# Kernel optimization log

Measured on AMD Instinct MI355X. Metric: run time of the kernel, lower is better.

Reference implementation:

```python
import jax, jax.numpy as jnp
import numpy as np

B, S, E, H = 2, 2048, 2048, 16
D = E // H  # head_dim = 128
ROPE_BASE = 10000.0


def setup_inputs() -> dict:
    key = jax.random.key(0)
    ks = jax.random.split(key, 6)
    x = jax.random.normal(ks[0], (B, S, E), dtype=jnp.float32)
    # additive causal mask: 0 where attendable, -1e9 above diagonal
    causal = jnp.where(jnp.tril(jnp.ones((S, S), dtype=bool)), 0.0, -1e9).astype(jnp.float32)
    mask = jnp.broadcast_to(causal[None, None], (B, 1, S, S))
    # RoPE tables (rotate-half convention)
    inv_freq = 1.0 / (ROPE_BASE ** (jnp.arange(0, D, 2, dtype=jnp.float32) / D))
    freqs = jnp.arange(S, dtype=jnp.float32)[:, None] * inv_freq[None, :]  # [S, D/2]
    emb = jnp.concatenate([freqs, freqs], axis=-1)  # [S, D]
    cos, sin = jnp.cos(emb), jnp.sin(emb)
    std = 0.02
    Wq = jax.random.normal(ks[1], (E, E), dtype=jnp.float32) * std
    Wk = jax.random.normal(ks[2], (E, E), dtype=jnp.float32) * std
    Wv = jax.random.normal(ks[3], (E, E), dtype=jnp.float32) * std
    Wo = jax.random.normal(ks[4], (E, E), dtype=jnp.float32) * std
    zb = jnp.zeros((E,), dtype=jnp.float32)
    return {"x": x, "mask": mask, "cos": cos, "sin": sin,
            "Wq": Wq, "bq": zb, "Wk": Wk, "bk": zb, "Wv": Wv, "bv": zb,
            "Wo": Wo, "bo": zb, "rope_exclude": 0}


def _rotate_half(t):
    t1, t2 = jnp.split(t, 2, axis=-1)
    return jnp.concatenate([-t2, t1], axis=-1)


def _apply_rope(t, cos, sin, rope_exclude):
    # t: [B, H, S, D]; cos/sin: [S, D]
    rot = t * cos[None, None] + _rotate_half(t) * sin[None, None]
    keep = (jnp.arange(t.shape[2]) < rope_exclude)[None, None, :, None]
    return jnp.where(keep, t, rot)


def reference(x, mask, cos, sin, Wq, bq, Wk, bk, Wv, bv, Wo, bo, rope_exclude):
    b, s, e = x.shape
    scale = D ** -0.5
    def heads(y):
        return y.reshape(b, s, H, D).transpose(0, 2, 1, 3)  # [B,H,S,D]
    q = heads(x @ Wq.T + bq)
    k = heads(x @ Wk.T + bk)
    v = heads(x @ Wv.T + bv)
    q = _apply_rope(q, cos, sin, rope_exclude)
    k = _apply_rope(k, cos, sin, rope_exclude)
    scores = jnp.einsum('bhqd,bhkd->bhqk', q, k) * scale + mask
    attn = jax.nn.softmax(scores, axis=-1)  # dropout is identity in eval mode
    ctx = jnp.einsum('bhqk,bhkd->bhqd', attn, v)
    ctx = ctx.transpose(0, 2, 1, 3).reshape(b, s, e)
    return ctx @ Wo.T + bo
```

## Files before the change

### kernel.cpp

```cpp
#include <hip/hip_runtime.h>


#define BB 2
#define SS 2048
#define EE 2048
#define HH 16
#define DD 128
#define BH 32
#define MR 4096
#define BKK 64
#define NTK (EE / BKK)

typedef __attribute__((ext_vector_type(8))) short short8;
typedef __attribute__((ext_vector_type(4))) short short4v;
typedef __attribute__((ext_vector_type(4))) float floatx4;
typedef unsigned int u32;

__device__ __forceinline__ float bf2f(unsigned short u) {
    union { unsigned int i; float f; } v; v.i = ((unsigned int)u) << 16; return v.f;
}
__device__ __forceinline__ unsigned short f2bf(float f) {
    union { float f; unsigned int i; } v; v.f = f;
    unsigned int x = v.i;
    return (unsigned short)((x + 0x7fffu + ((x >> 16) & 1u)) >> 16);
}

__device__ __forceinline__ void async_copy16(const unsigned short* g, unsigned short* l) {
    __builtin_amdgcn_global_load_lds((const __attribute__((address_space(1))) u32*)g,
                                     (__attribute__((address_space(3))) u32*)l, 16, 0, 0);
}

__global__ __launch_bounds__(256)
void cvt_all(const float* __restrict__ x,  const float* __restrict__ Wq,
             const float* __restrict__ Wk, const float* __restrict__ Wv,
             const float* __restrict__ Wo, unsigned short* __restrict__ dst)
{
    const size_t wsz = (size_t)EE * EE;
    size_t i = ((size_t)blockIdx.x * 256 + threadIdx.x) * 8;
    const float* src; size_t off;
    if      (i <     wsz) { src = Wo; off = 0; }
    else if (i < 2 * wsz) { src = Wq; off = wsz; }
    else if (i < 3 * wsz) { src = Wk; off = 2 * wsz; }
    else if (i < 4 * wsz) { src = Wv; off = 3 * wsz; }
    else                  { src = x;  off = 4 * wsz; }
    const float* p = src + (i - off);
    floatx4 v0 = *(const floatx4*)p;
    floatx4 v1 = *(const floatx4*)(p + 4);
    short8 o;
    #pragma unroll
    for (int j = 0; j < 4; ++j) { o[j] = (short)f2bf(v0[j]); o[4 + j] = (short)f2bf(v1[j]); }
    *(short8*)&dst[i] = o;
}

__device__ __forceinline__ void stageA(const unsigned short* __restrict__ X,
                                       unsigned short* Asb, int mbase, int k0,
                                       int w, int lane)
{
    const int rsub = lane >> 3;
    const int ksw  = ((lane & 7) ^ rsub) << 3;
    #pragma unroll
    for (int h = 0; h < 2; ++h)
        #pragma unroll
        for (int c = 0; c < 2; ++c) {
            int r = h * 128 + (w * 2 + c) * 8 + rsub;
            async_copy16(&X[(size_t)(mbase + r) * EE + k0 + ksw],
                         &Asb[h * 8192 + (w * 2 + c) * 512]);
        }
}
__device__ __forceinline__ void stageB(const unsigned short* __restrict__ W,
                                       unsigned short* Bsb, int nbase, int k0,
                                       int w, int lane)
{
    const int rsub = lane >> 3;
    const int ksw  = ((lane & 7) ^ rsub) << 3;
    #pragma unroll
    for (int c = 0; c < 2; ++c) {
        int r = (w * 2 + c) * 8 + rsub;
        async_copy16(&W[(size_t)(nbase + r) * EE + k0 + ksw],
                     &Bsb[(w * 2 + c) * 512]);
    }
}

template<int MODE>
__global__ __launch_bounds__(512, 1)
void gemm8(const unsigned short* __restrict__ X,
           const unsigned short* __restrict__ W,
           const float* __restrict__ bias0,
           const float* __restrict__ bias1,
           const float* __restrict__ bias2,
           const float* __restrict__ cosT,
           const float* __restrict__ sinT,
           const int* __restrict__ rex,
           void* __restrict__ outv)
{
    __shared__ __align__(16) unsigned short As[3][256 * 64];
    __shared__ __align__(16) unsigned short Bs[3][128 * 64];

    const int NXB = (MODE == 0) ? 48 : 16;
    const int nwg = (MODE == 0) ? 768 : 256;
    const int q8  = nwg >> 3;
    const int wg  = ((int)blockIdx.x & 7) * q8 + ((int)blockIdx.x >> 3);
    const int xb = wg % NXB, yb = wg / NXB;
    const int mbase = yb * 256;
    const int nbase = xb * 128;

    const int tid  = threadIdx.x;
    const int w    = tid >> 6, lane = tid & 63;
    const int quad = lane >> 4, l16 = lane & 15;
    const int wm = w >> 1, wn = w & 1;

    floatx4 acc[4][4];
    #pragma unroll
    for (int mi = 0; mi < 4; ++mi)
        #pragma unroll
        for (int ni = 0; ni < 4; ++ni)
            acc[mi][ni] = (floatx4){0.f, 0.f, 0.f, 0.f};

    const int kx0 = (quad * 8) ^ ((l16 & 7) << 3);
    const int kx1 = (32 + quad * 8) ^ ((l16 & 7) << 3);

    stageA(X, As[0], mbase, 0,   w, lane);  stageB(W, Bs[0], nbase, 0,   w, lane);
    stageA(X, As[1], mbase, BKK, w, lane);  stageB(W, Bs[1], nbase, BKK, w, lane);
    asm volatile("s_waitcnt vmcnt(6)" ::: "memory");
    asm volatile("s_barrier" ::: "memory");

    for (int t = 0; t < NTK; ++t) {
        const unsigned short* Ab = As[t % 3];
        const unsigned short* Bb = Bs[t % 3];
        unsigned short* An = As[(t + 2) % 3];
        unsigned short* Bn = Bs[(t + 2) % 3];
        const bool pf = (t + 2 < NTK);
        const int kn = (t + 2) * BKK;

        short8 b[4][2];
        #pragma unroll
        for (int ni = 0; ni < 4; ++ni) {
            int rb = (wn * 64 + ni * 16 + l16) * 64;
            b[ni][0] = *(const short8*)&Bb[rb + kx0];
            b[ni][1] = *(const short8*)&Bb[rb + kx1];
        }
        short8 a[4][2];
        #pragma unroll
        for (int mi = 0; mi < 2; ++mi) {
            int ra = (wm * 64 + mi * 16 + l16) * 64;
            a[mi][0] = *(const short8*)&Ab[ra + kx0];
            a[mi][1] = *(const short8*)&Ab[ra + kx1];
        }
        if (pf) stageA(X, An, mbase, kn, w, lane);
        __builtin_amdgcn_s_setprio(1);
        #pragma unroll
        for (int mi = 0; mi < 2; ++mi)
            #pragma unroll
            for (int ni = 0; ni < 4; ++ni) {
                acc[mi][ni] = __builtin_amdgcn_mfma_f32_16x16x32_bf16(a[mi][0], b[ni][0], acc[mi][ni], 0, 0, 0);
                acc[mi][ni] = __builtin_amdgcn_mfma_f32_16x16x32_bf16(a[mi][1], b[ni][1], acc[mi][ni], 0, 0, 0);
            }
        __builtin_amdgcn_s_setprio(0);

        #pragma unroll
        for (int mi = 2; mi < 4; ++mi) {
            int ra = (wm * 64 + mi * 16 + l16) * 64;
            a[mi][0] = *(const short8*)&Ab[ra + kx0];
            a[mi][1] = *(const short8*)&Ab[ra + kx1];
        }
        if (pf) stageB(W, Bn, nbase, kn, w, lane);
        __builtin_amdgcn_s_setprio(1);
        #pragma unroll
        for (int mi = 2; mi < 4; ++mi)
            #pragma unroll
            for (int ni = 0; ni < 4; ++ni) {
                acc[mi][ni] = __builtin_amdgcn_mfma_f32_16x16x32_bf16(a[mi][0], b[ni][0], acc[mi][ni], 0, 0, 0);
                acc[mi][ni] = __builtin_amdgcn_mfma_f32_16x16x32_bf16(a[mi][1], b[ni][1], acc[mi][ni], 0, 0, 0);
            }
        __builtin_amdgcn_s_setprio(0);
        if (pf) asm volatile("s_waitcnt vmcnt(6)" ::: "memory");
        else    asm volatile("s_waitcnt vmcnt(0)" ::: "memory");
        asm volatile("s_barrier" ::: "memory");
    }

    if (MODE == 1) {
        #pragma unroll
        for (int ni = 0; ni < 4; ++ni) {
            int n = nbase + wn * 64 + ni * 16 + l16;
            float bval = bias0[n];
            #pragma unroll
            for (int mi = 0; mi < 4; ++mi)
                #pragma unroll
                for (int rr = 0; rr < 4; ++rr) {
                    int m = mbase + wm * 64 + mi * 16 + quad * 4 + rr;
                    ((float*)outv)[(size_t)m * EE + n] = acc[mi][ni][rr] + bval;
                }
        }
    } else {
        unsigned short (*Ls)[132] = (unsigned short(*)[132])&As[0][0];
        #pragma unroll
        for (int ni = 0; ni < 4; ++ni) {
            int nl = wn * 64 + ni * 16 + l16;
            int n  = nbase + nl;
            const float* bp = (n < 2048) ? bias0 : (n < 4096) ? bias1 : bias2;
            float bval = bp[n & (EE - 1)];
            #pragma unroll
            for (int mi = 0; mi < 4; ++mi)
                #pragma unroll
                for (int rr = 0; rr < 4; ++rr)
                    Ls[wm * 64 + mi * 16 + quad * 4 + rr][nl] = f2bf(acc[mi][ni][rr] + bval);
        }
        __syncthreads();

        const int r0 = tid >> 4;
        const int c0 = (tid & 15) * 4;
        const int nz = nbase + c0;
        const int z  = nz >> 11;
        const int hh = (nz >> 7) & (HH - 1);
        const float qs = (z == 0) ? 0.08838834764831845f : 1.0f;
        const int rexv = rex[0];
        unsigned short* op16 = (unsigned short*)outv;
        #pragma unroll
        for (int rr2 = 0; rr2 < 8; ++rr2) {
            int row = r0 * 8 + rr2;
            int m = mbase + row;
            int s = m & (SS - 1), bi = m >> 11;
            short4v lo = *(short4v*)&Ls[row][c0];
            short4v hi = *(short4v*)&Ls[row][c0 + 64];
            floatx4 c1 = *(const floatx4*)&cosT[(size_t)s * DD + c0];
            floatx4 s1 = *(const floatx4*)&sinT[(size_t)s * DD + c0];
            floatx4 c2 = *(const floatx4*)&cosT[(size_t)s * DD + c0 + 64];
            floatx4 s2 = *(const floatx4*)&sinT[(size_t)s * DD + c0 + 64];
            bool rot = (z < 2) && (s >= rexv);
            short4v o1, o2;
            #pragma unroll
            for (int c = 0; c < 4; ++c) {
                float f1 = bf2f((unsigned short)lo[c]);
                float f2 = bf2f((unsigned short)hi[c]);
                float r1 = rot ? (f1 * c1[c] - f2 * s1[c]) : f1;
                float r2 = rot ? (f2 * c2[c] + f1 * s2[c]) : f2;
                o1[c] = (short)f2bf(r1 * qs);
                o2[c] = (short)f2bf(r2 * qs);
            }
            size_t base = (size_t)z * ((size_t)BH * SS * DD)
                        + ((size_t)(bi * HH + hh) * SS + s) * DD;
            *(short4v*)&op16[base + c0]      = o1;
            *(short4v*)&op16[base + c0 + 64] = o2;
        }
    }
}

template<int MODE>
__global__ __launch_bounds__(256, 2)
void gemm_bt(const void* __restrict__ Xv,
             const float* __restrict__ W0,
             const float* __restrict__ W1,
             const float* __restrict__ W2,
             const float* __restrict__ bias0,
             const float* __restrict__ bias1,
             const float* __restrict__ bias2,
             void* __restrict__ outv)
{
    const float* W;
    const float* bias;
    unsigned short* op16 = nullptr;
    float* op32 = nullptr;
    if (MODE == 0) {
        int z = blockIdx.z;
        W    = (z == 0) ? W0 : (z == 1) ? W1 : W2;
        bias = (z == 0) ? bias0 : (z == 1) ? bias1 : bias2;
        op16 = (unsigned short*)outv + (size_t)z * ((size_t)BH * SS * DD);
    } else {
        W = W0; bias = bias0; op32 = (float*)outv;
    }

    __shared__ unsigned short As[4][128][8];
    __shared__ unsigned short Bs[4][128][8];

    const int tid  = threadIdx.x;
    const int wave = tid >> 6, lane = tid & 63;
    const int quad = lane >> 4, l16 = lane & 15;
    const int wr = (wave >> 1) * 64;
    const int wc = (wave & 1) * 64;
    const int mbase = blockIdx.y * 128, nbase = blockIdx.x * 128;

    const int srow  = tid >> 1;
    const int shalf = tid & 1;
    const int sc0   = shalf * 2;

    floatx4 acc[4][4];
    #pragma unroll
    for (int i = 0; i < 4; ++i)
        #pragma unroll
        for (int c = 0; c < 4; ++c)
            acc[i][c] = (floatx4){0.f, 0.f, 0.f, 0.f};

    const size_t arow = (size_t)(mbase + srow) * EE;
    const size_t brow = (size_t)(nbase + srow) * EE;

    for (int k0 = 0; k0 < EE; k0 += 32) {
        if (MODE == 0) {
            const float* px = &((const float*)Xv)[arow + k0 + shalf * 16];
            short8 lo, hi;
            #pragma unroll
            for (int j = 0; j < 8; ++j) lo[j] = (short)f2bf(px[j]);
            #pragma unroll
            for (int j = 0; j < 8; ++j) hi[j] = (short)f2bf(px[8 + j]);
            *(short8*)&As[sc0    ][srow][0] = lo;
            *(short8*)&As[sc0 + 1][srow][0] = hi;
        } else {
            const unsigned short* Xb = (const unsigned short*)Xv;
            *(short8*)&As[sc0    ][srow][0] = *(const short8*)&Xb[arow + k0 + shalf * 16];
            *(short8*)&As[sc0 + 1][srow][0] = *(const short8*)&Xb[arow + k0 + shalf * 16 + 8];
        }
        {
            const float* pw = &W[brow + k0 + shalf * 16];
            short8 lo, hi;
            #pragma unroll
            for (int j = 0; j < 8; ++j) lo[j] = (short)f2bf(pw[j]);
            #pragma unroll
            for (int j = 0; j < 8; ++j) hi[j] = (short)f2bf(pw[8 + j]);
            *(short8*)&Bs[sc0    ][srow][0] = lo;
            *(short8*)&Bs[sc0 + 1][srow][0] = hi;
        }
        __syncthreads();

        short8 a[4], b[4];
        #pragma unroll
        for (int i = 0; i < 4; ++i) a[i] = *(short8*)&As[quad][wr + i * 16 + l16][0];
        #pragma unroll
        for (int c = 0; c < 4; ++c) b[c] = *(short8*)&Bs[quad][wc + c * 16 + l16][0];
        #pragma unroll
        for (int i = 0; i < 4; ++i)
            #pragma unroll
            for (int c = 0; c < 4; ++c)
                acc[i][c] = __builtin_amdgcn_mfma_f32_16x16x32_bf16(a[i], b[c], acc[i][c], 0, 0, 0);
        __syncthreads();
    }

    #pragma unroll
    for (int c = 0; c < 4; ++c) {
        int n = nbase + wc + c * 16 + l16;
        float bval = bias[n];
        #pragma unroll
        for (int i = 0; i < 4; ++i) {
            #pragma unroll
            for (int r = 0; r < 4; ++r) {
                int m = mbase + wr + i * 16 + quad * 4 + r;
                float val = acc[i][c][r] + bval;
                if (MODE == 0) {
                    int bi = m >> 11, s = m & (SS - 1);
                    int h  = n >> 7,  d = n & (DD - 1);
                    op16[(((size_t)(bi * HH + h)) * SS + s) * DD + d] = f2bf(val);
                } else {
                    op32[(size_t)m * EE + n] = val;
                }
            }
        }
    }
}

__global__ __launch_bounds__(256)
void rope_kernel(unsigned short* __restrict__ Qw, unsigned short* __restrict__ Kw,
                 const float* __restrict__ cosT,
                 const float* __restrict__ sinT,
                 const int* __restrict__ rex)
{
    int idx = blockIdx.x * 256 + threadIdx.x;
    int d4 = idx & 15;
    int s  = (idx >> 4) & (SS - 1);
    int bh = (idx >> 15) & (BH - 1);
    int t  = idx >> 20;
    unsigned short* T = t ? Kw : Qw;
    const float qs = t ? 1.0f : 0.08838834764831845f;

    size_t base  = ((size_t)bh * SS + s) * DD + d4 * 4;
    size_t cbase = (size_t)s * DD + d4 * 4;

    short4v v1 = *(short4v*)&T[base];
    short4v v2 = *(short4v*)&T[base + 64];
    floatx4 c1 = *(const floatx4*)&cosT[cbase];
    floatx4 s1 = *(const floatx4*)&sinT[cbase];
    floatx4 c2 = *(const floatx4*)&cosT[cbase + 64];
    floatx4 s2 = *(const floatx4*)&sinT[cbase + 64];

    bool keep = (s < rex[0]);
    short4v o1, o2;
    #pragma unroll
    for (int i = 0; i < 4; ++i) {
        float f1 = bf2f((unsigned short)v1[i]);
        float f2 = bf2f((unsigned short)v2[i]);
        float r1 = f1 * c1[i] - f2 * s1[i];
        float r2 = f2 * c2[i] + f1 * s2[i];
        o1[i] = (short)f2bf((keep ? f1 : r1) * qs);
        o2[i] = (short)f2bf((keep ? f2 : r2) * qs);
    }
    *(short4v*)&T[base]      = o1;
    *(short4v*)&T[base + 64] = o2;
}

__global__ __launch_bounds__(512, 1)
void attn_mfma(const unsigned short* __restrict__ Qw,
               const unsigned short* __restrict__ Kw,
               const unsigned short* __restrict__ Vw,
               unsigned short* __restrict__ O)
{
    __shared__ unsigned short Ks[16][64][8];
    __shared__ unsigned short Vt[128][72];
    __shared__ unsigned short Ps[8][32][72];

    const int tid  = threadIdx.x;
    const int w    = tid >> 6, lane = tid & 63;
    const int quad = lane >> 4, l16 = lane & 15;
    const int bh = blockIdx.y;
    const int b = bh >> 4, h = bh & (HH - 1);
    const int x = blockIdx.x;
    const int half = w >> 2, wsub = w & 3;
    const int qbh  = half ? x : (15 - x);
    const int myrow = qbh * 128 + wsub * 32;

    const size_t head = (size_t)bh * SS * DD;

    short8 aq[2][4];
    #pragma unroll
    for (int hh = 0; hh < 2; ++hh) {
        const unsigned short* qp = &Qw[head + (size_t)(myrow + hh * 16 + l16) * DD];
        #pragma unroll
        for (int kc = 0; kc < 4; ++kc) aq[hh][kc] = *(const short8*)&qp[kc * 32 + quad * 8];
    }

    floatx4 oacc[2][8];
    #pragma unroll
    for (int hh = 0; hh < 2; ++hh)
        #pragma unroll
        for (int i = 0; i < 8; ++i) oacc[hh][i] = (floatx4){0.f, 0.f, 0.f, 0.f};
    float l_part[2][4];
    #pragma unroll
    for (int hh = 0; hh < 2; ++hh)
        #pragma unroll
        for (int r = 0; r < 4; ++r) l_part[hh][r] = 0.f;

    const int ntiles = 2 * (15 - x) + 2;
    for (int kt = 0; kt < ntiles; ++kt) {
        __syncthreads();

        #pragma unroll
        for (int it = 0; it < 2; ++it) {
            int key = it * 32 + (tid >> 4);
            int dc  = tid & 15;
            short8 v = *(const short8*)&Kw[head + (size_t)(kt * 64 + key) * DD + dc * 8];
            *(short8*)&Ks[dc][key ^ (dc & 7)][0] = v;
        }
        #pragma unroll
        for (int it = 0; it < 2; ++it) {
            int key = lane;
            int dc  = it * 8 + w;
            short8 v = *(const short8*)&Vw[head + (size_t)(kt * 64 + key) * DD + dc * 8];
            #pragma unroll
            for (int i = 0; i < 8; ++i) Vt[dc * 8 + i][key] = (unsigned short)v[i];
        }
        __syncthreads();

        if (kt * 64 > myrow + 31) continue;

        floatx4 sacc[2][4];
        #pragma unroll
        for (int hh = 0; hh < 2; ++hh)
            #pragma unroll
            for (int nt = 0; nt < 4; ++nt) sacc[hh][nt] = (floatx4){0.f, 0.f, 0.f, 0.f};
        #pragma unroll
        for (int kc = 0; kc < 4; ++kc) {
            int dcr = kc * 4 + quad;
            #pragma unroll
            for (int nt = 0; nt < 4; ++nt) {
                short8 bfrag = *(const short8*)&Ks[dcr][(nt * 16) + (l16 ^ (dcr & 7))][0];
                sacc[0][nt] = __builtin_amdgcn_mfma_f32_16x16x32_bf16(aq[0][kc], bfrag, sacc[0][nt], 0, 0, 0);
                sacc[1][nt] = __builtin_amdgcn_mfma_f32_16x16x32_bf16(aq[1][kc], bfrag, sacc[1][nt], 0, 0, 0);
            }
        }

        #pragma unroll
        for (int hh = 0; hh < 2; ++hh)
            #pragma unroll
            for (int nt = 0; nt < 4; ++nt)
                #pragma unroll
                for (int rr = 0; rr < 4; ++rr) {
                    int keyg = kt * 64 + nt * 16 + l16;
                    int qg   = myrow + hh * 16 + quad * 4 + rr;
                    float p = (keyg <= qg) ? __expf(sacc[hh][nt][rr]) : 0.f;
                    l_part[hh][rr] += p;
                    Ps[w][hh * 16 + quad * 4 + rr][nt * 16 + l16] = f2bf(p);
                }

        #pragma unroll
        for (int kc = 0; kc < 2; ++kc) {
            short8 pa0 = *(const short8*)&Ps[w][l16][kc * 32 + quad * 8];
            short8 pa1 = *(const short8*)&Ps[w][16 + l16][kc * 32 + quad * 8];
            #pragma unroll
            for (int nt = 0; nt < 8; ++nt) {
                short8 vb = *(const short8*)&Vt[nt * 16 + l16][kc * 32 + quad * 8];
                oacc[0][nt] = __builtin_amdgcn_mfma_f32_16x16x32_bf16(pa0, vb, oacc[0][nt], 0, 0, 0);
                oacc[1][nt] = __builtin_amdgcn_mfma_f32_16x16x32_bf16(pa1, vb, oacc[1][nt], 0, 0, 0);
            }
        }
    }

    #pragma unroll
    for (int hh = 0; hh < 2; ++hh)
        #pragma unroll
        for (int rr = 0; rr < 4; ++rr) {
            float l = l_part[hh][rr];
            l += __shfl_xor(l, 1, 16);
            l += __shfl_xor(l, 2, 16);
            l += __shfl_xor(l, 4, 16);
            l += __shfl_xor(l, 8, 16);
            float inv = 1.f / l;
            int qg = myrow + hh * 16 + quad * 4 + rr;
            unsigned short* cp = &O[((size_t)b * SS + qg) * EE + h * DD];
            #pragma unroll
            for (int nt = 0; nt < 8; ++nt)
                cp[nt * 16 + l16] = f2bf(oacc[hh][nt][rr] * inv);
        }
}

__global__ void sentinel_kernel(float* out, int n) {
    int i = blockIdx.x * 256 + threadIdx.x;
    if (i < n) out[i] = 1.0e6f;
}

extern "C" void kernel_launch(void* const* d_in, const int* in_sizes, int n_in,
                              void* d_out, int out_size, void* d_ws, size_t ws_size,
                              hipStream_t stream)
{
    const float* x    = (const float*)d_in[0];
    const float* cosT = (const float*)d_in[2];
    const float* sinT = (const float*)d_in[3];
    const float* Wq = (const float*)d_in[4];
    const float* bq = (const float*)d_in[5];
    const float* Wk = (const float*)d_in[6];
    const float* bk = (const float*)d_in[7];
    const float* Wv = (const float*)d_in[8];
    const float* bv = (const float*)d_in[9];
    const float* Wo = (const float*)d_in[10];
    const float* bo = (const float*)d_in[11];
    const int* rex = (const int*)d_in[12];

    const size_t tsz = (size_t)BH * SS * DD;
    const size_t wsz = (size_t)EE * EE;
    const size_t need_small = 4 * tsz * sizeof(unsigned short);
    const size_t need_big   = (3 * tsz + 4 * wsz + tsz) * sizeof(unsigned short);

    unsigned short* ws = (unsigned short*)d_ws;
    unsigned short* Qws = ws;
    unsigned short* Kws = ws + tsz;
    unsigned short* Vws = ws + 2 * tsz;

    if (ws_size >= need_big) {
        unsigned short* Wob = ws + 3 * tsz;
        unsigned short* Wqb = Wob + wsz;
        unsigned short* Wkb = Wqb + wsz;
        unsigned short* Wvb = Wkb + wsz;
        unsigned short* Xb  = Wvb + wsz;
        unsigned short* Cws = Xb;

        cvt_all<<<(int)((4 * wsz + tsz) / 8 / 256), 256, 0, stream>>>(x, Wq, Wk, Wv, Wo, Wob);

        gemm8<0><<<768, 512, 0, stream>>>(Xb, Wqb, bq, bk, bv, cosT, sinT, rex, Qws);
        attn_mfma<<<dim3(8, BH), 512, 0, stream>>>(Qws, Kws, Vws, Cws);
        gemm8<1><<<256, 512, 0, stream>>>(Cws, Wob, bo, bo, bo, cosT, sinT, rex, d_out);
    } else if (ws_size >= need_small) {
        unsigned short* Cws = ws + 3 * tsz;
        gemm_bt<0><<<dim3(16, 32, 3), 256, 0, stream>>>(x, Wq, Wk, Wv, bq, bk, bv, Qws);
        rope_kernel<<<8192, 256, 0, stream>>>(Qws, Kws, cosT, sinT, rex);
        attn_mfma<<<dim3(8, BH), 512, 0, stream>>>(Qws, Kws, Vws, Cws);
        gemm_bt<1><<<dim3(16, 32, 1), 256, 0, stream>>>(Cws, Wo, Wo, Wo, bo, bo, bo, d_out);
    } else {
        sentinel_kernel<<<(out_size + 255) / 256, 256, 0, stream>>>((float*)d_out, out_size);
    }
}
```

Baseline: 419.3 us.

## Double-buffer K/V tiles in attention with register prefetch and MFMA priority

The attention kernel now keeps two LDS buffers for K and V. The next tile's global loads are issued into registers before computing on the current tile, and are written to the other buffer afterwards, so one barrier per iteration replaces two. This is meant to hide global load latency behind the QK and PV MFMA work. It also raises wave priority around the MFMA sections with s_setprio. The cost is double the LDS for K/V and extra live registers for the prefetched data.

Result: no change. 411.1 us (-1.9%).

```diff
diff --git a/kernel.cpp b/kernel.cpp
--- a/kernel.cpp
+++ b/kernel.cpp
@@ -400,8 +400,8 @@
                const unsigned short* __restrict__ Vw,
                unsigned short* __restrict__ O)
 {
-    __shared__ unsigned short Ks[16][64][8];
-    __shared__ unsigned short Vt[128][72];
+    __shared__ unsigned short Ks[2][16][64][8];
+    __shared__ unsigned short Vt[2][128][72];
     __shared__ unsigned short Ps[8][32][72];
 
     const int tid  = threadIdx.x;
@@ -416,6 +416,9 @@
 
     const size_t head = (size_t)bh * SS * DD;
 
+    const int skdc  = tid & 15;
+    const int skrow = tid >> 4;
+
     short8 aq[2][4];
     #pragma unroll
     for (int hh = 0; hh < 2; ++hh) {
@@ -436,68 +439,94 @@
         for (int r = 0; r < 4; ++r) l_part[hh][r] = 0.f;
 
     const int ntiles = 2 * (15 - x) + 2;
+
+    short8 kreg[2], vreg[2];
+    #pragma unroll
+    for (int it = 0; it < 2; ++it)
+        kreg[it] = *(const short8*)&Kw[head + (size_t)(it * 32 + skrow) * DD + skdc * 8];
+    #pragma unroll
+    for (int it = 0; it < 2; ++it)
+        vreg[it] = *(const short8*)&Vw[head + (size_t)lane * DD + (it * 8 + w) * 8];
+    #pragma unroll
+    for (int it = 0; it < 2; ++it)
+        *(short8*)&Ks[0][skdc][(it * 32 + skrow) ^ (skdc & 7)][0] = kreg[it];
+    #pragma unroll
+    for (int it = 0; it < 2; ++it)
+        #pragma unroll
+        for (int i = 0; i < 8; ++i) Vt[0][(it * 8 + w) * 8 + i][lane] = (unsigned short)vreg[it][i];
+    __syncthreads();
+
     for (int kt = 0; kt < ntiles; ++kt) {
+        const int cur = kt & 1, nxt = cur ^ 1;
+        const bool pf = (kt + 1 < ntiles);
+
+        if (pf) {
+            const size_t koff = head + (size_t)((kt + 1) * 64) * DD;
+            #pragma unroll
+            for (int it = 0; it < 2; ++it)
+                kreg[it] = *(const short8*)&Kw[koff + (size_t)(it * 32 + skrow) * DD + skdc * 8];
+            #pragma unroll
+            for (int it = 0; it < 2; ++it)
+                vreg[it] = *(const short8*)&Vw[koff + (size_t)lane * DD + (it * 8 + w) * 8];
+        }
+
+        if (kt * 64 <= myrow + 31) {
+            floatx4 sacc[2][4];
+            #pragma unroll
+            for (int hh = 0; hh < 2; ++hh)
+                #pragma unroll
+                for (int nt = 0; nt < 4; ++nt) sacc[hh][nt] = (floatx4){0.f, 0.f, 0.f, 0.f};
+            __builtin_amdgcn_s_setprio(1);
+            #pragma unroll
+            for (int kc = 0; kc < 4; ++kc) {
+                int dcr = kc * 4 + quad;
+                #pragma unroll
+                for (int nt = 0; nt < 4; ++nt) {
+                    short8 bfrag = *(const short8*)&Ks[cur][dcr][(nt * 16) + (l16 ^ (dcr & 7))][0];
+                    sacc[0][nt] = __builtin_amdgcn_mfma_f32_16x16x32_bf16(aq[0][kc], bfrag, sacc[0][nt], 0, 0, 0);
+                    sacc[1][nt] = __builtin_amdgcn_mfma_f32_16x16x32_bf16(aq[1][kc], bfrag, sacc[1][nt], 0, 0, 0);
+                }
+            }
+            __builtin_amdgcn_s_setprio(0);
+
+            #pragma unroll
+            for (int hh = 0; hh < 2; ++hh)
+                #pragma unroll
+                for (int nt = 0; nt < 4; ++nt)
+                    #pragma unroll
+                    for (int rr = 0; rr < 4; ++rr) {
+                        int keyg = kt * 64 + nt * 16 + l16;
+                        int qg   = myrow + hh * 16 + quad * 4 + rr;
+                        float p = (keyg <= qg) ? __expf(sacc[hh][nt][rr]) : 0.f;
+                        l_part[hh][rr] += p;
+                        Ps[w][hh * 16 + quad * 4 + rr][nt * 16 + l16] = f2bf(p);
+                    }
+
+            __builtin_amdgcn_s_setprio(1);
+            #pragma unroll
+            for (int kc = 0; kc < 2; ++kc) {
+                short8 pa0 = *(const short8*)&Ps[w][l16][kc * 32 + quad * 8];
+                short8 pa1 = *(const short8*)&Ps[w][16 + l16][kc * 32 + quad * 8];
+                #pragma unroll
+                for (int nt = 0; nt < 8; ++nt) {
+                    short8 vb = *(const short8*)&Vt[cur][nt * 16 + l16][kc * 32 + quad * 8];
+                    oacc[0][nt] = __builtin_amdgcn_mfma_f32_16x16x32_bf16(pa0, vb, oacc[0][nt], 0, 0, 0);
+                    oacc[1][nt] = __builtin_amdgcn_mfma_f32_16x16x32_bf16(pa1, vb, oacc[1][nt], 0, 0, 0);
+                }
+            }
+            __builtin_amdgcn_s_setprio(0);
+        }
+
+        if (pf) {
+            #pragma unroll
+            for (int it = 0; it < 2; ++it)
+                *(short8*)&Ks[nxt][skdc][(it * 32 + skrow) ^ (skdc & 7)][0] = kreg[it];
+            #pragma unroll
+            for (int it = 0; it < 2; ++it)
+                #pragma unroll
+                for (int i = 0; i < 8; ++i) Vt[nxt][(it * 8 + w) * 8 + i][lane] = (unsigned short)vreg[it][i];
+        }
         __syncthreads();
-
-        #pragma unroll
-        for (int it = 0; it < 2; ++it) {
-            int key = it * 32 + (tid >> 4);
-            int dc  = tid & 15;
-            short8 v = *(const short8*)&Kw[head + (size_t)(kt * 64 + key) * DD + dc * 8];
-            *(short8*)&Ks[dc][key ^ (dc & 7)][0] = v;
-        }
-        #pragma unroll
-        for (int it = 0; it < 2; ++it) {
-            int key = lane;
-            int dc  = it * 8 + w;
-            short8 v = *(const short8*)&Vw[head + (size_t)(kt * 64 + key) * DD + dc * 8];
-            #pragma unroll
-            for (int i = 0; i < 8; ++i) Vt[dc * 8 + i][key] = (unsigned short)v[i];
-        }
-        __syncthreads();
-
-        if (kt * 64 > myrow + 31) continue;
-
-        floatx4 sacc[2][4];
-        #pragma unroll
-        for (int hh = 0; hh < 2; ++hh)
-            #pragma unroll
-            for (int nt = 0; nt < 4; ++nt) sacc[hh][nt] = (floatx4){0.f, 0.f, 0.f, 0.f};
-        #pragma unroll
-        for (int kc = 0; kc < 4; ++kc) {
-            int dcr = kc * 4 + quad;
-            #pragma unroll
-            for (int nt = 0; nt < 4; ++nt) {
-                short8 bfrag = *(const short8*)&Ks[dcr][(nt * 16) + (l16 ^ (dcr & 7))][0];
-                sacc[0][nt] = __builtin_amdgcn_mfma_f32_16x16x32_bf16(aq[0][kc], bfrag, sacc[0][nt], 0, 0, 0);
-                sacc[1][nt] = __builtin_amdgcn_mfma_f32_16x16x32_bf16(aq[1][kc], bfrag, sacc[1][nt], 0, 0, 0);
-            }
-        }
-
-        #pragma unroll
-        for (int hh = 0; hh < 2; ++hh)
-            #pragma unroll
-            for (int nt = 0; nt < 4; ++nt)
-                #pragma unroll
-                for (int rr = 0; rr < 4; ++rr) {
-                    int keyg = kt * 64 + nt * 16 + l16;
-                    int qg   = myrow + hh * 16 + quad * 4 + rr;
-                    float p = (keyg <= qg) ? __expf(sacc[hh][nt][rr]) : 0.f;
-                    l_part[hh][rr] += p;
-                    Ps[w][hh * 16 + quad * 4 + rr][nt * 16 + l16] = f2bf(p);
-                }
-
-        #pragma unroll
-        for (int kc = 0; kc < 2; ++kc) {
-            short8 pa0 = *(const short8*)&Ps[w][l16][kc * 32 + quad * 8];
-            short8 pa1 = *(const short8*)&Ps[w][16 + l16][kc * 32 + quad * 8];
-            #pragma unroll
-            for (int nt = 0; nt < 8; ++nt) {
-                short8 vb = *(const short8*)&Vt[nt * 16 + l16][kc * 32 + quad * 8];
-                oacc[0][nt] = __builtin_amdgcn_mfma_f32_16x16x32_bf16(pa0, vb, oacc[0][nt], 0, 0, 0);
-                oacc[1][nt] = __builtin_amdgcn_mfma_f32_16x16x32_bf16(pa1, vb, oacc[1][nt], 0, 0, 0);
-            }
-        }
     }
 
     #pragma unroll
```
